# Performance work log

Measured on AMD Instinct MI355X. Metric: run time of the kernel, lower is better.

## Reference

```python
import jax, jax.numpy as jnp
import numpy as np
from jax import lax

# Config (matches init_kwargs): TrajGRU per HKO-7 reference impl (Shi et al.)
B, T, Cin, H, W = 8, 12, 1, 128, 128
F_, L = 64, 5            # out_channels (hidden filters), num trajectories
h_, w_ = H // 2, W // 2  # post-downsample spatial size


def _conv(x, w, b, stride=1, pad=0):
    y = lax.conv_general_dilated(x, w, (stride, stride), [(pad, pad), (pad, pad)],
                                 dimension_numbers=('NCHW', 'OIHW', 'NCHW'))
    return y + b[None, :, None, None]


def _leaky(x):
    return jnp.where(x >= 0, x, 0.2 * x)  # LeakyReLU(0.2)


def _warp_multi(img, flows):
    # img: (B,C,h,w); flows: (B,L,2,h,w) pixel displacements.
    # Bilinear grid_sample with zero padding; the HKO normalization
    # (2*v/(W-1)-1) followed by align_corners=True denormalization is the
    # identity, so we sample directly at grid + flow in pixel space.
    Bb, C, Hh, Ww = img.shape
    x = jnp.arange(Ww, dtype=img.dtype)[None, None, None, :] + flows[:, :, 0]  # (B,L,h,w)
    y = jnp.arange(Hh, dtype=img.dtype)[None, None, :, None] + flows[:, :, 1]
    x0 = jnp.floor(x); y0 = jnp.floor(y)
    x1 = x0 + 1.0;     y1 = y0 + 1.0
    imgl = img.transpose(0, 2, 3, 1)  # (B,h,w,C)
    bidx = jnp.arange(Bb)[:, None, None, None]

    def gather(xi, yi):
        valid = (xi >= 0) & (xi <= Ww - 1) & (yi >= 0) & (yi <= Hh - 1)
        xic = jnp.clip(xi, 0, Ww - 1).astype(jnp.int32)
        yic = jnp.clip(yi, 0, Hh - 1).astype(jnp.int32)
        return imgl[bidx, yic, xic] * valid[..., None].astype(img.dtype)  # (B,L,h,w,C)

    wa = ((x1 - x) * (y1 - y))[..., None]
    wb = ((x1 - x) * (y - y0))[..., None]
    wc = ((x - x0) * (y1 - y))[..., None]
    wd = ((x - x0) * (y - y0))[..., None]
    out = wa * gather(x0, y0) + wb * gather(x0, y1) + wc * gather(x1, y0) + wd * gather(x1, y1)
    # concat L warped copies along channels: (B,L,h,w,C) -> (B, L*C, h, w)
    return out.transpose(0, 1, 4, 2, 3).reshape(Bb, L * C, Hh, Ww)


def setup_inputs() -> dict:
    key = jax.random.key(0)
    ks = jax.random.split(key, 13)
    def rn(k, shape, s=0.05):
        return jax.random.normal(k, shape, dtype=jnp.float32) * s
    return {
        'x': jax.random.normal(ks[0], (B, T, Cin, H, W), dtype=jnp.float32),
        'W_down': rn(ks[1], (F_ * T, Cin * T, 4, 4)),
        'b_down': rn(ks[2], (F_ * T,)),
        'W_i2h': rn(ks[3], (3 * F_, F_, 3, 3)),
        'b_i2h': rn(ks[4], (3 * F_,)),
        'W_i2f': rn(ks[5], (32, F_, 5, 5)),
        'b_i2f': rn(ks[6], (32,)),
        'W_h2f': rn(ks[7], (32, F_, 5, 5)),
        'b_h2f': rn(ks[8], (32,)),
        'W_flow': rn(ks[9], (2 * L, 32, 5, 5), 0.02),
        'b_flow': rn(ks[10], (2 * L,), 0.02),
        'W_ret': rn(ks[11], (3 * F_, L * F_, 1, 1)),
        'b_ret': rn(ks[12], (3 * F_,)),
    }


def reference(x, W_down, b_down, W_i2h, b_i2h, W_i2f, b_i2f, W_h2f, b_h2f,
              W_flow, b_flow, W_ret, b_ret):
    Bb = x.shape[0]
    # downsample conv (k=4,s=2,p=1) + LeakyReLU(0.2) on time-stacked channels
    xd = _leaky(_conv(x.reshape(Bb, T * Cin, H, W), W_down, b_down, stride=2, pad=1))
    seq = xd.reshape(Bb, T, F_, h_, w_).transpose(1, 0, 2, 3, 4)  # (T,B,F,h,w)

    # input-dependent convs are batched across all timesteps up front
    flat = seq.reshape(T * Bb, F_, h_, w_)
    i2h_all = _conv(flat, W_i2h, b_i2h, pad=1).reshape(T, Bb, 3 * F_, h_, w_)
    i2f_all = _conv(flat, W_i2f, b_i2f, pad=2).reshape(T, Bb, 32, h_, w_)

    def step(hprev, inp):
        i2h_t, i2f_t = inp
        # flow generator: leaky(i2f(x_t) + h2f(h)) -> flows conv -> L 2-ch flows
        f1 = _leaky(i2f_t + _conv(hprev, W_h2f, b_h2f, pad=2))
        flows = _conv(f1, W_flow, b_flow, pad=2).reshape(Bb, L, 2, h_, w_)
        warped = _warp_multi(hprev, -flows)          # (B, L*F, h, w)
        h2h = _conv(warped, W_ret, b_ret)            # 1x1 projection -> (B, 3F, h, w)
        ir, iu, im = jnp.split(i2h_t, 3, axis=1)
        hr, hu, hm = jnp.split(h2h, 3, axis=1)
        r = jax.nn.sigmoid(ir + hr)
        u = jax.nn.sigmoid(iu + hu)
        m = _leaky(im + r * hm)
        hnew = u * hprev + (1.0 - u) * m
        return hnew, hnew

    h0 = jnp.zeros((Bb, F_, h_, w_), x.dtype)
    _, outs = lax.scan(step, h0, (i2h_all, i2f_all))  # (T,B,F,h,w)
    return outs.transpose(1, 0, 2, 3, 4)              # (B,T,F,h,w)
```

## Files before the change

### kernel.cpp

```cpp
#include <hip/hip_runtime.h>
#include <cstdint>

typedef long long ll;
typedef __bf16 bf16x8 __attribute__((ext_vector_type(8)));
typedef float f32x4 __attribute__((ext_vector_type(4)));
typedef unsigned int u32x4 __attribute__((ext_vector_type(4)));

#define NB 8
#define NT 12
#define NF 64
#define HWSZ 4096

struct alignas(8)  bh4 { __bf16 h[4]; };
struct alignas(16) bh8 { __bf16 h[8]; };

static __device__ inline f32x4 mfma16(bf16x8 a, bf16x8 b, f32x4 c) {
  return __builtin_amdgcn_mfma_f32_16x16x32_bf16(a, b, c, 0, 0, 0);
}
static __device__ inline bf16x8 ld8(const __bf16* p) {
  u32x4 u = *(const u32x4*)p;
  return __builtin_bit_cast(bf16x8, u);
}
static __device__ inline void st4(__bf16* p, float a0, float a1, float a2, float a3) {
  bh4 t; t.h[0] = (__bf16)a0; t.h[1] = (__bf16)a1; t.h[2] = (__bf16)a2; t.h[3] = (__bf16)a3;
  *(bh4*)p = t;
}
static __device__ inline float lky(float a) { return a >= 0.f ? a : 0.2f * a; }

static __device__ inline int swz_bid() {
  int bid = blockIdx.x;
  return ((gridDim.x & 7) == 0) ? (bid & 7) * (gridDim.x >> 3) + (bid >> 3) : bid;
}

template<int W, int HALO>
static __device__ void stage8(__bf16* dst, const __bf16* grow) {
  int tid = threadIdx.x;
  u32x4 zz = {0u, 0u, 0u, 0u};
  #pragma unroll
  for (int it = 0; it < 2; ++it) {
    int i = tid + it * 256;
    int xr = i >> 3, g = i & 7, xi = xr + HALO;
    u32x4 v = zz;
    if (grow) v = *(const u32x4*)(grow + xr * 64 + g * 8);
    *(u32x4*)(dst + (g * W + xi) * 8) = v;
  }
  if (tid < 16 * HALO) {
    int h = tid >> 3, g = tid & 7;
    int xi = (h < HALO) ? h : 64 + h;
    *(u32x4*)(dst + (g * W + xi) * 8) = zz;
  }
}

template<int W, int HALO>
static __device__ void stage4(__bf16* dst, const __bf16* grow) {
  int tid = threadIdx.x;
  u32x4 zz = {0u, 0u, 0u, 0u};
  {
    int xr = tid >> 2, g = tid & 3, xi = xr + HALO;
    u32x4 v = zz;
    if (grow) v = *(const u32x4*)(grow + xr * 32 + g * 8);
    *(u32x4*)(dst + (g * W + xi) * 8) = v;
  }
  if (tid < 8 * HALO) {
    int h = tid >> 2, g = tid & 3;
    int xi = (h < HALO) ? h : 64 + h;
    *(u32x4*)(dst + (g * W + xi) * 8) = zz;
  }
}

__global__ __launch_bounds__(256) void k_prep(
    const float* __restrict__ Wd, const float* __restrict__ Wc,
    const float* __restrict__ Wi, const float* __restrict__ Wh,
    const float* __restrict__ Wfl, const float* __restrict__ Wret,
    __bf16* __restrict__ Adown, __bf16* __restrict__ Ai2h,
    __bf16* __restrict__ Afi, __bf16* __restrict__ Afh,
    __bf16* __restrict__ Afl, __bf16* __restrict__ Aret) {
  int n = blockIdx.x * 256 + threadIdx.x;
  if (n < 147456) {
    Adown[n] = (__bf16)Wd[n];
  } else if (n < 258048) {
    int i = n - 147456;
    int tap = i / 12288, o = (i % 12288) / 64, c = i % 64;
    Ai2h[i] = (__bf16)Wc[(o * 64 + c) * 9 + tap];
  } else if (n < 309248) {
    int i = n - 258048;
    int tap = i / 2048, o = (i % 2048) / 64, c = i % 64;
    Afi[i] = (__bf16)Wi[(o * 64 + c) * 25 + tap];
  } else if (n < 360448) {
    int i = n - 309248;
    int tap = i / 2048, o = (i % 2048) / 64, c = i % 64;
    Afh[i] = (__bf16)Wh[(o * 64 + c) * 25 + tap];
  } else if (n < 373248) {
    int i = n - 360448;
    int tap = i / 512, o = (i % 512) / 32, c = i % 32;
    Afl[i] = (__bf16)(o < 10 ? Wfl[(o * 32 + c) * 25 + tap] : 0.f);
  } else if (n < 434688) {
    Aret[n - 373248] = (__bf16)Wret[n - 373248];
  }
}

__global__ __launch_bounds__(256) void k_down(
    const float* __restrict__ x, const __bf16* __restrict__ Adown,
    const float* __restrict__ bd, __bf16* __restrict__ seq) {
  __shared__ __bf16 smd[6240];
  int bi = swz_bid();
  int zQ = bi & 3, y = (bi >> 2) & 63, b = bi >> 8;
  int tid = threadIdx.x;
  for (int i = tid; i < 6240; i += 256) {
    int ic = i / 520, rem = i % 520, ky = rem / 130, xi = rem % 130;
    int ix = xi - 1, iy = 2 * y - 1 + ky;
    float v = (ix >= 0 && ix < 128 && iy >= 0 && iy < 128)
                  ? x[(((ll)(b * 12 + ic) * 128 + iy) << 7) + ix] : 0.f;
    smd[i] = (__bf16)v;
  }
  __syncthreads();
  int wv = __builtin_amdgcn_readfirstlane(tid >> 6);
  int lane = tid & 63, q = lane >> 4, lr = lane & 15;
  int px = wv * 16 + lr;
  f32x4 zv = {0.f, 0.f, 0.f, 0.f};
  f32x4 acc[12];
  #pragma unroll
  for (int mt = 0; mt < 12; ++mt) acc[mt] = zv;

  for (int ks = 0; ks < 6; ++ks) {
    int k0 = ks * 32 + q * 8;
    int ic = k0 >> 4, ky0 = (k0 >> 2) & 3;
    const __bf16* rp = smd + (ic * 4 + ky0) * 130 + 2 * px;
    bh8 bb;
    #pragma unroll
    for (int j = 0; j < 8; ++j)
      bb.h[j] = rp[(j >> 2) * 130 + (j & 3)];
    bf16x8 bfr = __builtin_bit_cast(bf16x8, bb);
    #pragma unroll
    for (int mt = 0; mt < 12; ++mt) {
      bf16x8 afr = ld8(Adown + ((ll)(zQ * 192 + mt * 16 + lr) * 192 + k0));
      acc[mt] = mfma16(afr, bfr, acc[mt]);
    }
  }
  #pragma unroll
  for (int mt = 0; mt < 12; ++mt) {
    int t_idx = zQ * 3 + (mt >> 2);
    int f0 = (mt & 3) * 16 + q * 4;
    float v[4];
    #pragma unroll
    for (int r = 0; r < 4; ++r)
      v[r] = lky(acc[mt][r] + bd[zQ * 192 + mt * 16 + q * 4 + r]);
    st4(seq + (((ll)(t_idx * NB + b) * 4096 + y * 64 + px) * 64 + f0),
        v[0], v[1], v[2], v[3]);
  }
}

__global__ __launch_bounds__(256, 2) void k_i2h4(
    const __bf16* __restrict__ in0, const __bf16* __restrict__ A,
    const float* __restrict__ bc, __bf16* __restrict__ out0) {
  __shared__ __align__(16) __bf16 smI[6 * 8 * 67 * 8];
  __shared__ __align__(16) __bf16 smA[2][96 * 64];
  int bi_ = swz_bid();
  int yg = bi_ & 15, och = (bi_ >> 4) & 1, tb = bi_ >> 5;
  int y0 = yg * 4;
  const __bf16* base = in0 + (ll)tb * (4096 * 64);
  const __bf16* Ab = A + ((ll)och * 96) * 64;
  int tid = threadIdx.x;
  #pragma unroll
  for (int s = 0; s < 6; ++s) {
    int yr = y0 - 1 + s;
    stage8<67, 1>(smI + s * (8 * 67 * 8),
                  (yr >= 0 && yr < 64) ? base + (ll)yr * 64 * 64 : nullptr);
  }
  u32x4 ar[3];
  auto loadA = [&](int tap) {
    #pragma unroll
    for (int it = 0; it < 3; ++it) {
      int j = it * 256 + tid;
      ar[it] = *(const u32x4*)(Ab + (ll)tap * (192 * 64) + j * 8);
    }
  };
  auto writeA = [&](int buf) {
    #pragma unroll
    for (int it = 0; it < 3; ++it) {
      int j = it * 256 + tid;
      int oc = j >> 3, g = j & 7;
      *(u32x4*)(smA[buf] + oc * 64 + ((g ^ (oc & 7)) * 8)) = ar[it];
    }
  };
  loadA(0);
  writeA(0);
  __syncthreads();

  int wv = __builtin_amdgcn_readfirstlane(tid >> 6);
  int lane = tid & 63, q = lane >> 4, lr = lane & 15;
  int mh = wv & 1, rg = wv >> 1;
  f32x4 zv = {0.f, 0.f, 0.f, 0.f};
  f32x4 acc[3][8];
  #pragma unroll
  for (int mt = 0; mt < 3; ++mt)
    #pragma unroll
    for (int nt = 0; nt < 8; ++nt) acc[mt][nt] = zv;

  for (int tap = 0; tap < 9; ++tap) {
    if (tap < 8) loadA(tap + 1);
    int ky = tap / 3, kx = tap % 3;
    const __bf16* Ax = smA[tap & 1];
    #pragma unroll
    for (int ks = 0; ks < 2; ++ks) {
      bf16x8 afr[3];
      #pragma unroll
      for (int mt = 0; mt < 3; ++mt) {
        int oc = mh * 48 + mt * 16 + lr;
        afr[mt] = ld8(Ax + oc * 64 + (((ks * 4 + q) ^ (lr & 7)) * 8));
      }
      bf16x8 bfr[8];
      #pragma unroll
      for (int rl = 0; rl < 2; ++rl)
        #pragma unroll
        for (int nx = 0; nx < 4; ++nx) {
          int s = rg * 2 + rl + ky;
          bfr[rl * 4 + nx] =
              ld8(smI + ((s * 8 + ks * 4 + q) * 67 + nx * 16 + lr + kx) * 8);
        }
      #pragma unroll
      for (int mt = 0; mt < 3; ++mt)
        #pragma unroll
        for (int nt = 0; nt < 8; ++nt)
          acc[mt][nt] = mfma16(afr[mt], bfr[nt], acc[mt][nt]);
    }
    if (tap < 8) writeA((tap + 1) & 1);
    __syncthreads();
  }

  #pragma unroll
  for (int rl = 0; rl < 2; ++rl)
    #pragma unroll
    for (int nx = 0; nx < 4; ++nx) {
      int row = y0 + rg * 2 + rl, px = nx * 16 + lr;
      __bf16* op = out0 + ((ll)tb * 4096 + row * 64 + px) * 192;
      #pragma unroll
      for (int mt = 0; mt < 3; ++mt) {
        int oc0 = och * 96 + mh * 48 + mt * 16 + q * 4;
        f32x4 a = acc[mt][rl * 4 + nx];
        st4(op + oc0, a[0] + bc[oc0], a[1] + bc[oc0 + 1],
                      a[2] + bc[oc0 + 2], a[3] + bc[oc0 + 3]);
      }
    }
}

__global__ __launch_bounds__(256, 2) void k_i2fb(
    const __bf16* __restrict__ in0, const __bf16* __restrict__ A,
    __bf16* __restrict__ out0) {
  __shared__ __align__(16) __bf16 smI[8 * 8 * 69 * 8];
  __shared__ __align__(16) __bf16 smA[2][32 * 64];
  float* red = (float*)smI;
  int bi_ = swz_bid();
  int yg = bi_ & 15, tb = bi_ >> 4;
  int y0 = yg * 4;
  const __bf16* base = in0 + (ll)tb * (4096 * 64);
  int tid = threadIdx.x;
  #pragma unroll
  for (int s = 0; s < 8; ++s) {
    int yr = y0 - 2 + s;
    stage8<69, 2>(smI + s * (8 * 69 * 8),
                  (yr >= 0 && yr < 64) ? base + (ll)yr * 64 * 64 : nullptr);
  }
  u32x4 ar;
  auto loadA = [&](int tap) { ar = *(const u32x4*)(A + (ll)tap * 2048 + tid * 8); };
  auto writeA = [&](int buf) {
    int oc = tid >> 3, g = tid & 7;
    *(u32x4*)(smA[buf] + oc * 64 + ((g ^ (oc & 7)) * 8)) = ar;
  };
  loadA(0);
  writeA(0);
  __syncthreads();

  int wv = __builtin_amdgcn_readfirstlane(tid >> 6);
  int lane = tid & 63, q = lane >> 4, lr = lane & 15;
  int rg = wv & 1, ksh = wv >> 1;
  f32x4 zv = {0.f, 0.f, 0.f, 0.f};
  f32x4 acc[2][8];
  #pragma unroll
  for (int mt = 0; mt < 2; ++mt)
    #pragma unroll
    for (int nt = 0; nt < 8; ++nt) acc[mt][nt] = zv;

  for (int tap = 0; tap < 25; ++tap) {
    if (tap < 24) loadA(tap + 1);
    int ky = tap / 5, kx = tap % 5;
    const __bf16* Ax = smA[tap & 1];
    bf16x8 afr[2];
    #pragma unroll
    for (int mt = 0; mt < 2; ++mt) {
      int oc = mt * 16 + lr;
      afr[mt] = ld8(Ax + oc * 64 + (((ksh * 4 + q) ^ (lr & 7)) * 8));
    }
    bf16x8 bfr[8];
    #pragma unroll
    for (int rl = 0; rl < 2; ++rl)
      #pragma unroll
      for (int nx = 0; nx < 4; ++nx) {
        int s = rg * 2 + rl + ky;
        bfr[rl * 4 + nx] =
            ld8(smI + ((s * 8 + ksh * 4 + q) * 69 + nx * 16 + lr + kx) * 8);
      }
    #pragma unroll
    for (int mt = 0; mt < 2; ++mt)
      #pragma unroll
      for (int nt = 0; nt < 8; ++nt)
        acc[mt][nt] = mfma16(afr[mt], bfr[nt], acc[mt][nt]);
    if (tap < 24) writeA((tap + 1) & 1);
    __syncthreads();
  }

  if (ksh == 1) {
    #pragma unroll
    for (int mt = 0; mt < 2; ++mt)
      #pragma unroll
      for (int rl = 0; rl < 2; ++rl)
        #pragma unroll
        for (int nx = 0; nx < 4; ++nx) {
          int row_l = rg * 2 + rl, px = nx * 16 + lr;
          int oc = mt * 16 + q * 4;
          f32x4 a = acc[mt][rl * 4 + nx];
          #pragma unroll
          for (int r = 0; r < 4; ++r)
            red[(row_l * 64 + px) * 33 + oc + r] = a[r];
        }
  }
  __syncthreads();
  if (ksh == 0) {
    #pragma unroll
    for (int mt = 0; mt < 2; ++mt)
      #pragma unroll
      for (int rl = 0; rl < 2; ++rl)
        #pragma unroll
        for (int nx = 0; nx < 4; ++nx) {
          int row_l = rg * 2 + rl, px = nx * 16 + lr;
          int oc0 = mt * 16 + q * 4;
          f32x4 a = acc[mt][rl * 4 + nx];
          float v[4];
          #pragma unroll
          for (int r = 0; r < 4; ++r)
            v[r] = a[r] + red[(row_l * 64 + px) * 33 + oc0 + r];
          st4(out0 + ((ll)tb * 4096 + (y0 + row_l) * 64 + px) * 32 + oc0,
              v[0], v[1], v[2], v[3]);
        }
  }
}

__global__ __launch_bounds__(256, 2) void k_h2f4(
    const __bf16* __restrict__ hb, const __bf16* __restrict__ A,
    const float* __restrict__ bi, const float* __restrict__ bh,
    const __bf16* __restrict__ i2f_t, __bf16* __restrict__ f1buf) {
  __shared__ __align__(16) __bf16 smI[5 * 8 * 69 * 8];
  float* red = (float*)smI;
  int bi_ = swz_bid();
  int y = bi_ & 63, b = bi_ >> 6;
  int tid = threadIdx.x;
  #pragma unroll
  for (int s = 0; s < 5; ++s) {
    int yr = y - 2 + s;
    stage8<69, 2>(smI + s * (8 * 69 * 8),
                  (yr >= 0 && yr < 64) ? hb + ((ll)(b * 64 + yr) * 64) * 64 : nullptr);
  }
  int wv = __builtin_amdgcn_readfirstlane(tid >> 6);
  int lane = tid & 63, q = lane >> 4, lr = lane & 15;

  bf16x8 apre[7][2][2];
  #pragma unroll
  for (int j = 0; j < 7; ++j) {
    int tap = 4 * j + wv;
    if (tap < 25) {
      #pragma unroll
      for (int ks = 0; ks < 2; ++ks)
        #pragma unroll
        for (int mt = 0; mt < 2; ++mt)
          apre[j][ks][mt] =
              ld8(A + ((ll)(tap * 32 + mt * 16 + lr) * 64 + ks * 32 + q * 8));
    }
  }
  __syncthreads();

  f32x4 zv = {0.f, 0.f, 0.f, 0.f};
  f32x4 acc[2][4];
  #pragma unroll
  for (int mt = 0; mt < 2; ++mt)
    #pragma unroll
    for (int nx = 0; nx < 4; ++nx) acc[mt][nx] = zv;

  #pragma unroll
  for (int j = 0; j < 7; ++j) {
    int tap = 4 * j + wv;
    if (tap < 25) {
      int ky = tap / 5, kx = tap % 5;
      #pragma unroll
      for (int ks = 0; ks < 2; ++ks) {
        bf16x8 bfr[4];
        #pragma unroll
        for (int nx = 0; nx < 4; ++nx)
          bfr[nx] = ld8(smI + ((ky * 8 + ks * 4 + q) * 69 + nx * 16 + lr + kx) * 8);
        #pragma unroll
        for (int mt = 0; mt < 2; ++mt)
          #pragma unroll
          for (int nx = 0; nx < 4; ++nx)
            acc[mt][nx] = mfma16(apre[j][ks][mt], bfr[nx], acc[mt][nx]);
      }
    }
  }
  __syncthreads();

  #pragma unroll
  for (int mt = 0; mt < 2; ++mt)
    #pragma unroll
    for (int nx = 0; nx < 4; ++nx) {
      int px = nx * 16 + lr, oc = mt * 16 + q * 4;
      f32x4 a = acc[mt][nx];
      #pragma unroll
      for (int r = 0; r < 4; ++r)
        red[wv * 2112 + px * 33 + oc + r] = a[r];
    }
  __syncthreads();

  int px = wv * 16 + (lane >> 2);
  int oc0 = (lane & 3) * 8;
  const __bf16* ip = i2f_t + ((ll)(b * 64 + y) * 64 + px) * 32 + oc0;
  bh8 iv = *(const bh8*)ip;
  bh8 ov;
  #pragma unroll
  for (int j = 0; j < 8; ++j) {
    float v = red[0 * 2112 + px * 33 + oc0 + j] + red[1 * 2112 + px * 33 + oc0 + j] +
              red[2 * 2112 + px * 33 + oc0 + j] + red[3 * 2112 + px * 33 + oc0 + j];
    ov.h[j] = (__bf16)lky(v + (float)iv.h[j] + bi[oc0 + j] + bh[oc0 + j]);
  }
  *(bh8*)(f1buf + ((ll)(b * 64 + y) * 64 + px) * 32 + oc0) = ov;
}

__global__ __launch_bounds__(256, 3) void k_fwr(
    const __bf16* __restrict__ f1buf, const __bf16* __restrict__ Afl,
    const float* __restrict__ bfl, const __bf16* __restrict__ hb,
    const __bf16* __restrict__ Aret, const float* __restrict__ br,
    const __bf16* __restrict__ i2h_t, const float* __restrict__ hprevf,
    int t0, float* __restrict__ outp, ll osb, __bf16* __restrict__ hbc) {
  __shared__ __align__(16) __bf16 pool[64 * 40 * 8];
  __shared__ float flows[64 * 17];
  __bf16* f1l = pool;
  __bf16* wrp = pool;

  int bi = swz_bid();
  int y = bi & 63, b = bi >> 6;
  int tid = threadIdx.x;
  int wv = __builtin_amdgcn_readfirstlane(tid >> 6);
  int lane = tid & 63, q = lane >> 4, lr = lane & 15;
  int px = wv * 16 + lr;

  #pragma unroll
  for (int r = 0; r < 5; ++r) {
    int yr = y - 2 + r;
    stage4<69, 2>(f1l + r * (4 * 69 * 8),
                  (yr >= 0 && yr < 64) ? f1buf + ((ll)(b * 64 + yr) * 64) * 32 : nullptr);
  }
  __syncthreads();

  f32x4 acc1 = {0.f, 0.f, 0.f, 0.f};
  #pragma unroll
  for (int tap = 0; tap < 25; ++tap) {
    int ky = tap / 5, kx = tap % 5;
    bf16x8 bfr = ld8(f1l + (((ky * 4 + q) * 69) + px + kx) * 8);
    bf16x8 afr = ld8(Afl + ((ll)(tap * 16 + lr) * 32 + q * 8));
    acc1 = mfma16(afr, bfr, acc1);
  }
  __syncthreads();
  #pragma unroll
  for (int r = 0; r < 4; ++r) {
    int oc = q * 4 + r;
    flows[px * 17 + oc] = acc1[r] + (oc < 10 ? bfl[oc] : 0.f);
  }
  __syncthreads();

  {
    int xw = tid & 63, cg = tid >> 6;
    const __bf16* hbb = hb + ((ll)b << 18);
    #pragma unroll
    for (int l = 0; l < 5; ++l) {
      float fx = flows[xw * 17 + 2 * l];
      float fy = flows[xw * 17 + 2 * l + 1];
      float pxf = (float)xw - fx, pyf = (float)y - fy;
      float x0f = floorf(pxf), y0f = floorf(pyf);
      int x0 = (int)x0f, y0 = (int)y0f, x1 = x0 + 1, y1 = y0 + 1;
      float dx = pxf - x0f, dy = pyf - y0f;
      bool vx0 = x0 >= 0 && x0 <= 63, vx1 = x1 >= 0 && x1 <= 63;
      bool vy0 = y0 >= 0 && y0 <= 63, vy1 = y1 >= 0 && y1 <= 63;
      float wA = (vx0 && vy0) ? (1.f - dx) * (1.f - dy) : 0.f;
      float wB = (vx0 && vy1) ? (1.f - dx) * dy : 0.f;
      float wC = (vx1 && vy0) ? dx * (1.f - dy) : 0.f;
      float wD = (vx1 && vy1) ? dx * dy : 0.f;
      int cx0 = min(max(x0, 0), 63), cx1 = min(max(x1, 0), 63);
      int cy0 = min(max(y0, 0), 63), cy1 = min(max(y1, 0), 63);
      int o00 = (cy0 * 64 + cx0) * 64, o10 = (cy1 * 64 + cx0) * 64;
      int o01 = (cy0 * 64 + cx1) * 64, o11 = (cy1 * 64 + cx1) * 64;
      #pragma unroll
      for (int it = 0; it < 2; ++it) {
        int cgp = cg + it * 4;
        int c0 = cgp * 8;
        bf16x8 aA = ld8(hbb + o00 + c0), aB = ld8(hbb + o10 + c0);
        bf16x8 aC = ld8(hbb + o01 + c0), aD = ld8(hbb + o11 + c0);
        bh8 ov;
        #pragma unroll
        for (int i = 0; i < 8; ++i)
          ov.h[i] = (__bf16)(wA * (float)aA[i] + wB * (float)aB[i] +
                             wC * (float)aC[i] + wD * (float)aD[i]);
        int G = l * 8 + cgp;
        int Gs = (G & ~7) | ((G & 7) ^ (xw & 7));
        *(bh8*)(wrp + (xw * 40 + Gs) * 8) = ov;
      }
    }
  }
  __syncthreads();

  f32x4 zv = {0.f, 0.f, 0.f, 0.f};
  f32x4 acc[12];
  #pragma unroll
  for (int mt = 0; mt < 12; ++mt) acc[mt] = zv;
  #pragma unroll
  for (int ks = 0; ks < 10; ++ks) {
    int Gr = ks * 4 + q;
    int Gs = (Gr & ~7) | ((Gr & 7) ^ (px & 7));
    bf16x8 bfr = ld8(wrp + (px * 40 + Gs) * 8);
    #pragma unroll
    for (int mt = 0; mt < 12; ++mt) {
      bf16x8 afr = ld8(Aret + ((ll)(mt * 16 + lr) * 320 + ks * 32 + q * 8));
      acc[mt] = mfma16(afr, bfr, acc[mt]);
    }
  }

  const __bf16* ih = i2h_t + ((ll)(b * 64 + y) * 64 + px) * 192;
  const float* hp = hprevf + (ll)b * osb + y * 64 + px;
  float* ob = outp + (ll)b * osb + y * 64 + px;
  __bf16* hc = hbc + ((ll)(b * 64 + y) * 64 + px) * 64;
  #pragma unroll
  for (int ft = 0; ft < 4; ++ft) {
    int f0 = ft * 16 + q * 4;
    bh4 irv = *(const bh4*)(ih + f0);
    bh4 iuv = *(const bh4*)(ih + f0 + 64);
    bh4 imv = *(const bh4*)(ih + f0 + 128);
    float hn4[4];
    #pragma unroll
    for (int r = 0; r < 4; ++r) {
      int f = f0 + r;
      float hr = acc[ft][r] + br[f];
      float hu = acc[ft + 4][r] + br[f + 64];
      float hm = acc[ft + 8][r] + br[f + 128];
      float rr = 1.f / (1.f + __expf(-((float)irv.h[r] + hr)));
      float uu = 1.f / (1.f + __expf(-((float)iuv.h[r] + hu)));
      float m = lky((float)imv.h[r] + rr * hm);
      float h0 = t0 ? 0.f : hp[(ll)f << 12];
      float hn = uu * h0 + (1.f - uu) * m;
      ob[(ll)f << 12] = hn;
      hn4[r] = hn;
    }
    st4(hc + f0, hn4[0], hn4[1], hn4[2], hn4[3]);
  }
}

extern "C" void kernel_launch(void* const* d_in, const int* in_sizes, int n_in,
                              void* d_out, int out_size, void* d_ws, size_t ws_size,
                              hipStream_t stream) {
  const float* x      = (const float*)d_in[0];
  const float* W_down = (const float*)d_in[1];
  const float* b_down = (const float*)d_in[2];
  const float* W_i2h  = (const float*)d_in[3];
  const float* b_i2h  = (const float*)d_in[4];
  const float* W_i2f  = (const float*)d_in[5];
  const float* b_i2f  = (const float*)d_in[6];
  const float* W_h2f  = (const float*)d_in[7];
  const float* b_h2f  = (const float*)d_in[8];
  const float* W_flow = (const float*)d_in[9];
  const float* b_flow = (const float*)d_in[10];
  const float* W_ret  = (const float*)d_in[11];
  const float* b_ret  = (const float*)d_in[12];
  float* out = (float*)d_out;

  const ll I2H_T = (ll)NB * 4096 * 192;
  const ll I2F_T = (ll)NB * 4096 * 32;
  const ll H_N   = (ll)NB * 4096 * 64;

  auto align256 = [](ll v) { return (v + 255) & ~255LL; };
  ll fixed = 0;
  fixed += align256(147456LL * 2);
  fixed += align256(110592LL * 2);
  fixed += align256(51200LL * 2);
  fixed += align256(51200LL * 2);
  fixed += align256(12800LL * 2);
  fixed += align256(61440LL * 2);
  fixed += align256((ll)NT * NB * 4096 * 64 * 2);
  fixed += align256((ll)NB * 4096 * 32 * 2);
  fixed += align256(H_N * 2) * 3;
  ll need_full = fixed + align256(NT * I2H_T * 2) + align256(NT * I2F_T * 2);
  int fits = (need_full <= (ll)ws_size);
  int slabT = fits ? NT : 1;

  char* p = (char*)d_ws;
  auto alloc = [&](ll bytes) { char* r = p; p += (bytes + 255) & ~255LL; return r; };
  __bf16* Adown  = (__bf16*)alloc(147456LL * 2);
  __bf16* Ai2h   = (__bf16*)alloc(110592LL * 2);
  __bf16* Afi    = (__bf16*)alloc(51200LL * 2);
  __bf16* Afh    = (__bf16*)alloc(51200LL * 2);
  __bf16* Afl    = (__bf16*)alloc(12800LL * 2);
  __bf16* Aret   = (__bf16*)alloc(61440LL * 2);
  __bf16* seq    = (__bf16*)alloc((ll)NT * NB * 4096 * 64 * 2);
  __bf16* f1buf  = (__bf16*)alloc((ll)NB * 4096 * 32 * 2);
  __bf16* hzb    = (__bf16*)alloc(H_N * 2);
  __bf16* hbufA  = (__bf16*)alloc(H_N * 2);
  __bf16* hbufB  = (__bf16*)alloc(H_N * 2);
  __bf16* i2h_sl = (__bf16*)alloc(slabT * I2H_T * 2);
  __bf16* i2f_sl = (__bf16*)alloc(slabT * I2F_T * 2);
  if (p > (char*)d_ws + ws_size) return;

  hipMemsetAsync(hzb, 0, (size_t)H_N * 2, stream);

  k_prep<<<1698, 256, 0, stream>>>(W_down, W_i2h, W_i2f, W_h2f, W_flow, W_ret,
                                   Adown, Ai2h, Afi, Afh, Afl, Aret);
  k_down<<<NB * 64 * 4, 256, 0, stream>>>(x, Adown, b_down, seq);

  if (fits) {
    k_i2h4<<<NT * NB * 2 * 16, 256, 0, stream>>>(seq, Ai2h, b_i2h, i2h_sl);
    k_i2fb<<<NT * NB * 16, 256, 0, stream>>>(seq, Afi, i2f_sl);
  }

  const ll osb = (ll)NT * NF * HWSZ;
  for (int t = 0; t < NT; ++t) {
    const __bf16* xt0 = seq + (ll)t * NB * 4096 * 64;
    if (!fits) {
      k_i2h4<<<NB * 2 * 16, 256, 0, stream>>>(xt0, Ai2h, b_i2h, i2h_sl);
      k_i2fb<<<NB * 16, 256, 0, stream>>>(xt0, Afi, i2f_sl);
    }
    int ti = fits ? t : 0;
    const __bf16* hb = (t == 0) ? hzb : ((t & 1) ? hbufA : hbufB);
    __bf16* hbc = (t & 1) ? hbufB : hbufA;
    const float* hpf = (t == 0) ? out : out + (ll)(t - 1) * NF * HWSZ;

    k_h2f4<<<NB * 64, 256, 0, stream>>>(hb, Afh, b_i2f, b_h2f,
                                        i2f_sl + (ll)ti * I2F_T, f1buf);
    k_fwr<<<NB * 64, 256, 0, stream>>>(f1buf, Afl, b_flow, hb, Aret, b_ret,
                                       i2h_sl + (ll)ti * I2H_T, hpf,
                                       (t == 0) ? 1 : 0,
                                       out + (ll)t * NF * HWSZ, osb, hbc);
  }
}
```

Before: 978.8 us.

## Split recurrent h2f and flow/warp kernels into half-row blocks for more parallelism

```diff
diff --git a/kernel.cpp b/kernel.cpp
--- a/kernel.cpp
+++ b/kernel.cpp
@@ -46,23 +46,6 @@
   }
   if (tid < 16 * HALO) {
     int h = tid >> 3, g = tid & 7;
-    int xi = (h < HALO) ? h : 64 + h;
-    *(u32x4*)(dst + (g * W + xi) * 8) = zz;
-  }
-}
-
-template<int W, int HALO>
-static __device__ void stage4(__bf16* dst, const __bf16* grow) {
-  int tid = threadIdx.x;
-  u32x4 zz = {0u, 0u, 0u, 0u};
-  {
-    int xr = tid >> 2, g = tid & 3, xi = xr + HALO;
-    u32x4 v = zz;
-    if (grow) v = *(const u32x4*)(grow + xr * 32 + g * 8);
-    *(u32x4*)(dst + (g * W + xi) * 8) = v;
-  }
-  if (tid < 8 * HALO) {
-    int h = tid >> 2, g = tid & 3;
     int xi = (h < HALO) ? h : 64 + h;
     *(u32x4*)(dst + (g * W + xi) * 8) = zz;
   }
@@ -345,63 +328,68 @@
   }
 }
 
-__global__ __launch_bounds__(256, 2) void k_h2f4(
+__global__ __launch_bounds__(256, 4) void k_h2f5(
     const __bf16* __restrict__ hb, const __bf16* __restrict__ A,
     const float* __restrict__ bi, const float* __restrict__ bh,
     const __bf16* __restrict__ i2f_t, __bf16* __restrict__ f1buf) {
-  __shared__ __align__(16) __bf16 smI[5 * 8 * 69 * 8];
+  __shared__ __align__(16) __bf16 smI[5 * 8 * 37 * 8];
   float* red = (float*)smI;
   int bi_ = swz_bid();
-  int y = bi_ & 63, b = bi_ >> 6;
+  int xh = bi_ & 1, y = (bi_ >> 1) & 63, b = bi_ >> 7;
+  int x0 = xh * 32;
   int tid = threadIdx.x;
-  #pragma unroll
-  for (int s = 0; s < 5; ++s) {
-    int yr = y - 2 + s;
-    stage8<69, 2>(smI + s * (8 * 69 * 8),
-                  (yr >= 0 && yr < 64) ? hb + ((ll)(b * 64 + yr) * 64) * 64 : nullptr);
+  u32x4 zz = {0u, 0u, 0u, 0u};
+  for (int i = tid; i < 5 * 296; i += 256) {
+    int s = i / 296, rem = i % 296, xi = rem >> 3, g = rem & 7;
+    int yr = y - 2 + s, xg = x0 - 2 + xi;
+    u32x4 v = zz;
+    if (yr >= 0 && yr < 64 && xg >= 0 && xg < 64)
+      v = *(const u32x4*)(hb + ((ll)(b * 64 + yr) * 64 + xg) * 64 + g * 8);
+    *(u32x4*)(smI + ((s * 8 + g) * 37 + xi) * 8) = v;
   }
   int wv = __builtin_amdgcn_readfirstlane(tid >> 6);
   int lane = tid & 63, q = lane >> 4, lr = lane & 15;
 
-  bf16x8 apre[7][2][2];
+  bf16x8 cur[2][2], nxt[2][2];
+  auto loadAt = [&](int tap, bf16x8 a[2][2]) {
+    #pragma unroll
+    for (int ks = 0; ks < 2; ++ks)
+      #pragma unroll
+      for (int mt = 0; mt < 2; ++mt)
+        a[ks][mt] = ld8(A + ((ll)(tap * 32 + mt * 16 + lr) * 64 + ks * 32 + q * 8));
+  };
+  loadAt(wv, cur);
+  __syncthreads();
+
+  f32x4 zv = {0.f, 0.f, 0.f, 0.f};
+  f32x4 acc[2][2];
+  #pragma unroll
+  for (int mt = 0; mt < 2; ++mt)
+    #pragma unroll
+    for (int nx = 0; nx < 2; ++nx) acc[mt][nx] = zv;
+
   #pragma unroll
   for (int j = 0; j < 7; ++j) {
     int tap = 4 * j + wv;
     if (tap < 25) {
-      #pragma unroll
-      for (int ks = 0; ks < 2; ++ks)
+      if (tap + 4 < 25) loadAt(tap + 4, nxt);
+      int ky = tap / 5, kx = tap % 5;
+      #pragma unroll
+      for (int ks = 0; ks < 2; ++ks) {
+        bf16x8 bfr[2];
         #pragma unroll
-        for (int mt = 0; mt < 2; ++mt)
-          apre[j][ks][mt] =
-              ld8(A + ((ll)(tap * 32 + mt * 16 + lr) * 64 + ks * 32 + q * 8));
-    }
-  }
-  __syncthreads();
-
-  f32x4 zv = {0.f, 0.f, 0.f, 0.f};
-  f32x4 acc[2][4];
-  #pragma unroll
-  for (int mt = 0; mt < 2; ++mt)
-    #pragma unroll
-    for (int nx = 0; nx < 4; ++nx) acc[mt][nx] = zv;
-
-  #pragma unroll
-  for (int j = 0; j < 7; ++j) {
-    int tap = 4 * j + wv;
-    if (tap < 25) {
-      int ky = tap / 5, kx = tap % 5;
-      #pragma unroll
-      for (int ks = 0; ks < 2; ++ks) {
-        bf16x8 bfr[4];
-        #pragma unroll
-        for (int nx = 0; nx < 4; ++nx)
-          bfr[nx] = ld8(smI + ((ky * 8 + ks * 4 + q) * 69 + nx * 16 + lr + kx) * 8);
+        for (int nx = 0; nx < 2; ++nx)
+          bfr[nx] = ld8(smI + ((ky * 8 + ks * 4 + q) * 37 + nx * 16 + lr + kx) * 8);
         #pragma unroll
         for (int mt = 0; mt < 2; ++mt)
           #pragma unroll
-          for (int nx = 0; nx < 4; ++nx)
-            acc[mt][nx] = mfma16(apre[j][ks][mt], bfr[nx], acc[mt][nx]);
+          for (int nx = 0; nx < 2; ++nx)
+            acc[mt][nx] = mfma16(cur[ks][mt], bfr[nx], acc[mt][nx]);
       }
+      #pragma unroll
+      for (int ks = 0; ks < 2; ++ks)
+        #pragma unroll
+        for (int mt = 0; mt < 2; ++mt) cur[ks][mt] = nxt[ks][mt];
     }
   }
   __syncthreads();
@@ -409,154 +397,174 @@
   #pragma unroll
   for (int mt = 0; mt < 2; ++mt)
     #pragma unroll
-    for (int nx = 0; nx < 4; ++nx) {
-      int px = nx * 16 + lr, oc = mt * 16 + q * 4;
+    for (int nx = 0; nx < 2; ++nx) {
+      int pxl = nx * 16 + lr, oc = mt * 16 + q * 4;
       f32x4 a = acc[mt][nx];
       #pragma unroll
       for (int r = 0; r < 4; ++r)
-        red[wv * 2112 + px * 33 + oc + r] = a[r];
-    }
-  __syncthreads();
-
-  int px = wv * 16 + (lane >> 2);
-  int oc0 = (lane & 3) * 8;
-  const __bf16* ip = i2f_t + ((ll)(b * 64 + y) * 64 + px) * 32 + oc0;
-  bh8 iv = *(const bh8*)ip;
-  bh8 ov;
-  #pragma unroll
-  for (int j = 0; j < 8; ++j) {
-    float v = red[0 * 2112 + px * 33 + oc0 + j] + red[1 * 2112 + px * 33 + oc0 + j] +
-              red[2 * 2112 + px * 33 + oc0 + j] + red[3 * 2112 + px * 33 + oc0 + j];
-    ov.h[j] = (__bf16)lky(v + (float)iv.h[j] + bi[oc0 + j] + bh[oc0 + j]);
-  }
-  *(bh8*)(f1buf + ((ll)(b * 64 + y) * 64 + px) * 32 + oc0) = ov;
-}
-
-__global__ __launch_bounds__(256, 3) void k_fwr(
+        red[wv * 1056 + pxl * 33 + oc + r] = a[r];
+    }
+  __syncthreads();
+
+  int pxl = tid >> 3, oc0 = (tid & 7) * 4;
+  const __bf16* ip = i2f_t + ((ll)(b * 64 + y) * 64 + x0 + pxl) * 32 + oc0;
+  bh4 iv = *(const bh4*)ip;
+  float v[4];
+  #pragma unroll
+  for (int r = 0; r < 4; ++r) {
+    float s = red[0 * 1056 + pxl * 33 + oc0 + r] + red[1 * 1056 + pxl * 33 + oc0 + r] +
+              red[2 * 1056 + pxl * 33 + oc0 + r] + red[3 * 1056 + pxl * 33 + oc0 + r];
+    v[r] = lky(s + (float)iv.h[r] + bi[oc0 + r] + bh[oc0 + r]);
+  }
+  st4(f1buf + ((ll)(b * 64 + y) * 64 + x0 + pxl) * 32 + oc0, v[0], v[1], v[2], v[3]);
+}
+
+__global__ __launch_bounds__(256, 4) void k_fwr2(
     const __bf16* __restrict__ f1buf, const __bf16* __restrict__ Afl,
     const float* __restrict__ bfl, const __bf16* __restrict__ hb,
     const __bf16* __restrict__ Aret, const float* __restrict__ br,
     const __bf16* __restrict__ i2h_t, const float* __restrict__ hprevf,
     int t0, float* __restrict__ outp, ll osb, __bf16* __restrict__ hbc) {
-  __shared__ __align__(16) __bf16 pool[64 * 40 * 8];
-  __shared__ float flows[64 * 17];
-  __bf16* f1l = pool;
-  __bf16* wrp = pool;
+  __shared__ __align__(16) float exbuf[192 * 33];
+  __shared__ float flows[32 * 17];
+  __bf16* f1l = (__bf16*)exbuf;
+  __bf16* wrp = (__bf16*)exbuf;
 
   int bi = swz_bid();
-  int y = bi & 63, b = bi >> 6;
+  int xh = bi & 1, y = (bi >> 1) & 63, b = bi >> 7;
+  int x0 = xh * 32;
   int tid = threadIdx.x;
   int wv = __builtin_amdgcn_readfirstlane(tid >> 6);
   int lane = tid & 63, q = lane >> 4, lr = lane & 15;
-  int px = wv * 16 + lr;
-
-  #pragma unroll
-  for (int r = 0; r < 5; ++r) {
-    int yr = y - 2 + r;
-    stage4<69, 2>(f1l + r * (4 * 69 * 8),
-                  (yr >= 0 && yr < 64) ? f1buf + ((ll)(b * 64 + yr) * 64) * 32 : nullptr);
-  }
-  __syncthreads();
-
-  f32x4 acc1 = {0.f, 0.f, 0.f, 0.f};
-  #pragma unroll
-  for (int tap = 0; tap < 25; ++tap) {
-    int ky = tap / 5, kx = tap % 5;
-    bf16x8 bfr = ld8(f1l + (((ky * 4 + q) * 69) + px + kx) * 8);
-    bf16x8 afr = ld8(Afl + ((ll)(tap * 16 + lr) * 32 + q * 8));
-    acc1 = mfma16(afr, bfr, acc1);
-  }
-  __syncthreads();
-  #pragma unroll
-  for (int r = 0; r < 4; ++r) {
-    int oc = q * 4 + r;
-    flows[px * 17 + oc] = acc1[r] + (oc < 10 ? bfl[oc] : 0.f);
+
+  u32x4 zz = {0u, 0u, 0u, 0u};
+  for (int i = tid; i < 5 * 148; i += 256) {
+    int s = i / 148, rem = i % 148, xi = rem >> 2, g = rem & 3;
+    int yr = y - 2 + s, xg = x0 - 2 + xi;
+    u32x4 v = zz;
+    if (yr >= 0 && yr < 64 && xg >= 0 && xg < 64)
+      v = *(const u32x4*)(f1buf + ((ll)(b * 64 + yr) * 64 + xg) * 32 + g * 8);
+    *(u32x4*)(f1l + ((s * 4 + g) * 37 + xi) * 8) = v;
+  }
+  __syncthreads();
+
+  if (wv < 2) {
+    f32x4 acc1 = {0.f, 0.f, 0.f, 0.f};
+    #pragma unroll
+    for (int tap = 0; tap < 25; ++tap) {
+      int ky = tap / 5, kx = tap % 5;
+      bf16x8 bfr = ld8(f1l + ((ky * 4 + q) * 37 + wv * 16 + lr + kx) * 8);
+      bf16x8 afr = ld8(Afl + ((ll)(tap * 16 + lr) * 32 + q * 8));
+      acc1 = mfma16(afr, bfr, acc1);
+    }
+    #pragma unroll
+    for (int r = 0; r < 4; ++r) {
+      int oc = q * 4 + r;
+      flows[(wv * 16 + lr) * 17 + oc] = acc1[r] + (oc < 10 ? bfl[oc] : 0.f);
+    }
   }
   __syncthreads();
 
   {
-    int xw = tid & 63, cg = tid >> 6;
+    int pxl = tid & 31, cg = tid >> 5;
+    int xw = x0 + pxl;
     const __bf16* hbb = hb + ((ll)b << 18);
     #pragma unroll
     for (int l = 0; l < 5; ++l) {
-      float fx = flows[xw * 17 + 2 * l];
-      float fy = flows[xw * 17 + 2 * l + 1];
+      float fx = flows[pxl * 17 + 2 * l];
+      float fy = flows[pxl * 17 + 2 * l + 1];
       float pxf = (float)xw - fx, pyf = (float)y - fy;
       float x0f = floorf(pxf), y0f = floorf(pyf);
-      int x0 = (int)x0f, y0 = (int)y0f, x1 = x0 + 1, y1 = y0 + 1;
+      int xx0 = (int)x0f, yy0 = (int)y0f, xx1 = xx0 + 1, yy1 = yy0 + 1;
       float dx = pxf - x0f, dy = pyf - y0f;
-      bool vx0 = x0 >= 0 && x0 <= 63, vx1 = x1 >= 0 && x1 <= 63;
-      bool vy0 = y0 >= 0 && y0 <= 63, vy1 = y1 >= 0 && y1 <= 63;
+      bool vx0 = xx0 >= 0 && xx0 <= 63, vx1 = xx1 >= 0 && xx1 <= 63;
+      bool vy0 = yy0 >= 0 && yy0 <= 63, vy1 = yy1 >= 0 && yy1 <= 63;
       float wA = (vx0 && vy0) ? (1.f - dx) * (1.f - dy) : 0.f;
       float wB = (vx0 && vy1) ? (1.f - dx) * dy : 0.f;
       float wC = (vx1 && vy0) ? dx * (1.f - dy) : 0.f;
       float wD = (vx1 && vy1) ? dx * dy : 0.f;
-      int cx0 = min(max(x0, 0), 63), cx1 = min(max(x1, 0), 63);
-      int cy0 = min(max(y0, 0), 63), cy1 = min(max(y1, 0), 63);
+      int cx0 = min(max(xx0, 0), 63), cx1 = min(max(xx1, 0), 63);
+      int cy0 = min(max(yy0, 0), 63), cy1 = min(max(yy1, 0), 63);
       int o00 = (cy0 * 64 + cx0) * 64, o10 = (cy1 * 64 + cx0) * 64;
       int o01 = (cy0 * 64 + cx1) * 64, o11 = (cy1 * 64 + cx1) * 64;
-      #pragma unroll
-      for (int it = 0; it < 2; ++it) {
-        int cgp = cg + it * 4;
-        int c0 = cgp * 8;
-        bf16x8 aA = ld8(hbb + o00 + c0), aB = ld8(hbb + o10 + c0);
-        bf16x8 aC = ld8(hbb + o01 + c0), aD = ld8(hbb + o11 + c0);
-        bh8 ov;
-        #pragma unroll
-        for (int i = 0; i < 8; ++i)
-          ov.h[i] = (__bf16)(wA * (float)aA[i] + wB * (float)aB[i] +
-                             wC * (float)aC[i] + wD * (float)aD[i]);
-        int G = l * 8 + cgp;
-        int Gs = (G & ~7) | ((G & 7) ^ (xw & 7));
-        *(bh8*)(wrp + (xw * 40 + Gs) * 8) = ov;
-      }
+      int c0 = cg * 8;
+      bf16x8 aA = ld8(hbb + o00 + c0), aB = ld8(hbb + o10 + c0);
+      bf16x8 aC = ld8(hbb + o01 + c0), aD = ld8(hbb + o11 + c0);
+      bh8 ov;
+      #pragma unroll
+      for (int i = 0; i < 8; ++i)
+        ov.h[i] = (__bf16)(wA * (float)aA[i] + wB * (float)aB[i] +
+                           wC * (float)aC[i] + wD * (float)aD[i]);
+      int G = l * 8 + cg;
+      int Gs = (G & ~7) | ((G & 7) ^ (pxl & 7));
+      *(bh8*)(wrp + (pxl * 40 + Gs) * 8) = ov;
     }
   }
   __syncthreads();
 
   f32x4 zv = {0.f, 0.f, 0.f, 0.f};
-  f32x4 acc[12];
-  #pragma unroll
-  for (int mt = 0; mt < 12; ++mt) acc[mt] = zv;
+  f32x4 acc[3][2];
+  #pragma unroll
+  for (int mt = 0; mt < 3; ++mt)
+    #pragma unroll
+    for (int nt = 0; nt < 2; ++nt) acc[mt][nt] = zv;
   #pragma unroll
   for (int ks = 0; ks < 10; ++ks) {
-    int Gr = ks * 4 + q;
-    int Gs = (Gr & ~7) | ((Gr & 7) ^ (px & 7));
-    bf16x8 bfr = ld8(wrp + (px * 40 + Gs) * 8);
-    #pragma unroll
-    for (int mt = 0; mt < 12; ++mt) {
-      bf16x8 afr = ld8(Aret + ((ll)(mt * 16 + lr) * 320 + ks * 32 + q * 8));
-      acc[mt] = mfma16(afr, bfr, acc[mt]);
-    }
-  }
-
-  const __bf16* ih = i2h_t + ((ll)(b * 64 + y) * 64 + px) * 192;
-  const float* hp = hprevf + (ll)b * osb + y * 64 + px;
-  float* ob = outp + (ll)b * osb + y * 64 + px;
-  __bf16* hc = hbc + ((ll)(b * 64 + y) * 64 + px) * 64;
-  #pragma unroll
-  for (int ft = 0; ft < 4; ++ft) {
-    int f0 = ft * 16 + q * 4;
-    bh4 irv = *(const bh4*)(ih + f0);
-    bh4 iuv = *(const bh4*)(ih + f0 + 64);
-    bh4 imv = *(const bh4*)(ih + f0 + 128);
-    float hn4[4];
-    #pragma unroll
-    for (int r = 0; r < 4; ++r) {
-      int f = f0 + r;
-      float hr = acc[ft][r] + br[f];
-      float hu = acc[ft + 4][r] + br[f + 64];
-      float hm = acc[ft + 8][r] + br[f + 128];
-      float rr = 1.f / (1.f + __expf(-((float)irv.h[r] + hr)));
-      float uu = 1.f / (1.f + __expf(-((float)iuv.h[r] + hu)));
-      float m = lky((float)imv.h[r] + rr * hm);
-      float h0 = t0 ? 0.f : hp[(ll)f << 12];
-      float hn = uu * h0 + (1.f - uu) * m;
-      ob[(ll)f << 12] = hn;
-      hn4[r] = hn;
-    }
-    st4(hc + f0, hn4[0], hn4[1], hn4[2], hn4[3]);
-  }
+    bf16x8 bfr[2];
+    #pragma unroll
+    for (int nt = 0; nt < 2; ++nt) {
+      int pxl = nt * 16 + lr;
+      int Gr = ks * 4 + q;
+      int Gs = (Gr & ~7) | ((Gr & 7) ^ (pxl & 7));
+      bfr[nt] = ld8(wrp + (pxl * 40 + Gs) * 8);
+    }
+    #pragma unroll
+    for (int mt = 0; mt < 3; ++mt) {
+      bf16x8 afr = ld8(Aret + ((ll)((wv * 3 + mt) * 16 + lr) * 320 + ks * 32 + q * 8));
+      #pragma unroll
+      for (int nt = 0; nt < 2; ++nt)
+        acc[mt][nt] = mfma16(afr, bfr[nt], acc[mt][nt]);
+    }
+  }
+  __syncthreads();
+
+  #pragma unroll
+  for (int mt = 0; mt < 3; ++mt)
+    #pragma unroll
+    for (int nt = 0; nt < 2; ++nt) {
+      int oc = (wv * 3 + mt) * 16 + q * 4;
+      int pxl = nt * 16 + lr;
+      #pragma unroll
+      for (int r = 0; r < 4; ++r)
+        exbuf[(oc + r) * 33 + pxl] = acc[mt][nt][r];
+    }
+  __syncthreads();
+
+  int pxl = tid >> 3, f0 = (tid & 7) * 8;
+  int xg = x0 + pxl;
+  const __bf16* ih = i2h_t + ((ll)(b * 64 + y) * 64 + xg) * 192;
+  const float* hp = hprevf + (ll)b * osb + y * 64 + xg;
+  float* ob = outp + (ll)b * osb + y * 64 + xg;
+  __bf16* hc = hbc + ((ll)(b * 64 + y) * 64 + xg) * 64 + f0;
+  bh8 irv = *(const bh8*)(ih + f0);
+  bh8 iuv = *(const bh8*)(ih + 64 + f0);
+  bh8 imv = *(const bh8*)(ih + 128 + f0);
+  bh8 hv;
+  #pragma unroll
+  for (int j = 0; j < 8; ++j) {
+    int f = f0 + j;
+    float hr = exbuf[f * 33 + pxl] + br[f];
+    float hu = exbuf[(f + 64) * 33 + pxl] + br[f + 64];
+    float hm = exbuf[(f + 128) * 33 + pxl] + br[f + 128];
+    float rr = 1.f / (1.f + __expf(-((float)irv.h[j] + hr)));
+    float uu = 1.f / (1.f + __expf(-((float)iuv.h[j] + hu)));
+    float m = lky((float)imv.h[j] + rr * hm);
+    float h0 = t0 ? 0.f : hp[(ll)f << 12];
+    float hn = uu * h0 + (1.f - uu) * m;
+    ob[(ll)f << 12] = hn;
+    hv.h[j] = (__bf16)hn;
+  }
+  *(bh8*)hc = hv;
 }
 
 extern "C" void kernel_launch(void* const* d_in, const int* in_sizes, int n_in,
@@ -636,11 +644,11 @@
     __bf16* hbc = (t & 1) ? hbufB : hbufA;
     const float* hpf = (t == 0) ? out : out + (ll)(t - 1) * NF * HWSZ;
 
-    k_h2f4<<<NB * 64, 256, 0, stream>>>(hb, Afh, b_i2f, b_h2f,
-                                        i2f_sl + (ll)ti * I2F_T, f1buf);
-    k_fwr<<<NB * 64, 256, 0, stream>>>(f1buf, Afl, b_flow, hb, Aret, b_ret,
-                                       i2h_sl + (ll)ti * I2H_T, hpf,
-                                       (t == 0) ? 1 : 0,
-                                       out + (ll)t * NF * HWSZ, osb, hbc);
-  }
-}
+    k_h2f5<<<NB * 64 * 2, 256, 0, stream>>>(hb, Afh, b_i2f, b_h2f,
+                                            i2f_sl + (ll)ti * I2F_T, f1buf);
+    k_fwr2<<<NB * 64 * 2, 256, 0, stream>>>(f1buf, Afl, b_flow, hb, Aret, b_ret,
+                                            i2h_sl + (ll)ti * I2H_T, hpf,
+                                            (t == 0) ? 1 : 0,
+                                            out + (ll)t * NF * HWSZ, osb, hbc);
+  }
+}
```

Measured after the change: 884.5 us. 1.11x faster.
